# Kernel tuning notes

Hardware: AMD Instinct MI355X
Metric: run time of the kernel (lower is better)

The kernel has to match this reference:

```python
import jax, jax.numpy as jnp
import numpy as np
import math

E_IN, E_OUT = 512, 96
B, QL, PL = 64, 128, 196

def _lin(k, shape):
    fan_in = shape[1]
    bound = 1.0 / math.sqrt(fan_in)
    k1, k2 = jax.random.split(k)
    W = jax.random.uniform(k1, shape, jnp.float32, -bound, bound)
    b = jax.random.uniform(k2, (shape[0],), jnp.float32, -bound, bound)
    return W, b

def setup_inputs() -> dict:
    key = jax.random.key(0)
    ks = jax.random.split(key, 16)
    inp = {
        'z_d_cls': jax.random.normal(ks[0], (B, E_IN), jnp.float32),
        'Z_d_tok': jax.random.normal(ks[1], (B, QL, E_IN), jnp.float32),
        'z_t_cls': jax.random.normal(ks[2], (B, E_IN), jnp.float32),
        'Z_t_tok': jax.random.normal(ks[3], (B, QL, E_IN), jnp.float32),
        'z_v_cls': jax.random.normal(ks[4], (B, E_IN), jnp.float32),
        'Z_v_patch': jax.random.normal(ks[5], (B, PL, E_IN), jnp.float32),
    }
    names = ['t_cls', 'd_cls', 'v_cls', 't_tok', 'v_patch', 'tgl_q', 'tgl_k', 'tgl_v']
    for i, n in enumerate(names):
        W, b = _lin(ks[6 + i], (E_OUT, E_IN))
        inp[f'W_{n}'] = W
        inp[f'b_{n}'] = b
    inp['ln_g'] = jnp.ones((E_OUT,), jnp.float32)
    inp['ln_b'] = jnp.zeros((E_OUT,), jnp.float32)
    return inp

def _l2n(x, eps=1e-6):
    return x / jnp.maximum(jnp.linalg.norm(x, axis=-1, keepdims=True), eps)

def _proj(x, W, b):
    return x @ W.T + b

def _layer_norm(x, g, b, eps=1e-5):
    mu = jnp.mean(x, axis=-1, keepdims=True)
    var = jnp.mean((x - mu) ** 2, axis=-1, keepdims=True)
    return (x - mu) / jnp.sqrt(var + eps) * g + b

def reference(z_d_cls, Z_d_tok, z_t_cls, Z_t_tok, z_v_cls, Z_v_patch,
              W_t_cls, b_t_cls, W_d_cls, b_d_cls, W_v_cls, b_v_cls,
              W_t_tok, b_t_tok, W_v_patch, b_v_patch,
              W_tgl_q, b_tgl_q, W_tgl_k, b_tgl_k, W_tgl_v, b_tgl_v,
              ln_g, ln_b):
    # --- TGG: global-global text/doc cosine sim [B, B]
    t = _l2n(_proj(z_t_cls, W_t_cls, b_t_cls))
    d = _l2n(_proj(z_d_cls, W_d_cls, b_d_cls))
    S_TGG = t @ d.T
    # --- TGL: cross-attention over all batch pairs
    Q = _proj(Z_d_tok, W_tgl_q, b_tgl_q)   # [b, q, h]
    K = _proj(Z_t_tok, W_tgl_k, b_tgl_k)   # [c, k, h]
    V = _proj(Z_t_tok, W_tgl_v, b_tgl_v)   # [c, k, h]
    scores = jnp.einsum('bqh,ckh->bcqk', Q, K) / math.sqrt(E_OUT)
    attn = jax.nn.softmax(scores, axis=-1)
    context = jnp.einsum('bcqk,ckh->bcqh', attn, V).mean(axis=2)  # [b, c, h]
    context = _layer_norm(context, ln_g, ln_b)
    S_TGL = jnp.einsum('ih,ijh->ij', d, _l2n(context))
    S_TIB = 0.5 * (S_TGG + S_TGL)
    # --- CGG: global-global text/vision cosine sim
    v = _l2n(_proj(z_v_cls, W_v_cls, b_v_cls))
    S_CGG = t @ v.T
    # --- CLL: token-patch max similarity
    t_tok = _l2n(_proj(Z_t_tok, W_t_tok, b_t_tok))        # [b, t, h]
    v_pat = _l2n(_proj(Z_v_patch, W_v_patch, b_v_patch))  # [c, p, h]
    sim = jnp.einsum('bth,cph->bctp', t_tok, v_pat)
    S_CLL = sim.max(axis=(-1, -2))
    S_CAB = 0.5 * (S_CGG + S_CLL)
    return S_TIB + S_CAB
```

## Files before the change

kernel.cpp:

```cpp
#include <hip/hip_runtime.h>
#include <hip/hip_bf16.h>
#include <math.h>

typedef __bf16 bf16;
typedef __attribute__((ext_vector_type(8))) __bf16 bf16x8;
typedef __attribute__((ext_vector_type(2))) float f32x2;
typedef __attribute__((ext_vector_type(4))) float f32x4;
typedef __attribute__((ext_vector_type(4))) unsigned int uint4v;

#define MFMA16(a, b, c) __builtin_amdgcn_mfma_f32_16x16x32_bf16(a, b, c, 0, 0, 0)

#define QSCALE 0.14724450f

__device__ inline bf16x8 cvt8(const float* p) {
    f32x4 lo = *(const f32x4*)p;
    f32x4 hi = *(const f32x4*)(p + 4);
    bf16x8 r;
    r[0] = (bf16)lo[0]; r[1] = (bf16)lo[1]; r[2] = (bf16)lo[2]; r[3] = (bf16)lo[3];
    r[4] = (bf16)hi[0]; r[5] = (bf16)hi[1]; r[6] = (bf16)hi[2]; r[7] = (bf16)hi[3];
    return r;
}


struct WPtrs { const float* W[8]; };

__global__ __launch_bounds__(256) void cvtw_kernel(WPtrs wp, bf16* __restrict__ Wb) {
    int j   = blockIdx.x / 48;
    int blk = blockIdx.x - j * 48;
    int idx = (blk * 256 + threadIdx.x) * 4;
    f32x4 v = *(const f32x4*)(wp.W[j] + idx);
    bf16* dst = Wb + j * 49152 + idx;
    dst[0] = (bf16)v[0]; dst[1] = (bf16)v[1]; dst[2] = (bf16)v[2]; dst[3] = (bf16)v[3];
}


struct ProjParams {
    const float* src[8];
    const float* B[8];
    void* dst[8];
    const bf16* Wb;
};

__global__ __launch_bounds__(256) void proj_kernel(ProjParams p) {
    int g   = blockIdx.x;
    int tid = threadIdx.x;
    int w2 = tid >> 6;
    int nh = w2 & 1, kh = w2 >> 1;
    int lane = tid & 63;
    int m = lane & 15, quad = lane >> 4;

    int job = 0, base = 0;
    if (g >= 2)    { job = 1; base = 2; }
    if (g >= 4)    { job = 2; base = 4; }
    if (g >= 6)    { job = 3; base = 6; }
    if (g >= 262)  { job = 4; base = 262; }
    if (g >= 518)  { job = 5; base = 518; }
    if (g >= 774)  { job = 6; base = 774; }
    if (g >= 1030) { job = 7; base = 1030; }
    int r0 = (g - base) << 5;

    const float* X  = p.src[job];
    const bf16*  wb = p.Wb + job * 49152 + (size_t)(nh * 48 + m) * 512 + kh * 256 + quad * 8;
    const float* x0 = X + (size_t)(r0 + m) * 512 + kh * 256 + quad * 8;
    const float* x1 = x0 + 16 * 512;

    f32x4 acc[2][3] = {};
    #pragma unroll
    for (int kk = 0; kk < 256; kk += 32) {
        bf16x8 a0 = cvt8(x0 + kk);
        bf16x8 a1 = cvt8(x1 + kk);
        #pragma unroll
        for (int nt = 0; nt < 3; nt++) {
            bf16x8 b = *(const bf16x8*)(wb + nt * 8192 + kk);
            acc[0][nt] = MFMA16(a0, b, acc[0][nt]);
            acc[1][nt] = MFMA16(a1, b, acc[1][nt]);
        }
    }

    __shared__ float red[2 * 64 * 24];
    __shared__ float sx[2][2][16];
    float* myred = red + (nh * 64 + lane) * 24;
    if (kh) {
        #pragma unroll
        for (int t2 = 0; t2 < 2; t2++)
            #pragma unroll
            for (int nt = 0; nt < 3; nt++)
                *(f32x4*)(myred + (t2 * 3 + nt) * 4) = acc[t2][nt];
    }
    __syncthreads();

    bool norm = (job < 3) || (job >= 6);
    const float* Bv = p.B[job];
    if (!kh) {
        #pragma unroll
        for (int t2 = 0; t2 < 2; t2++)
            #pragma unroll
            for (int nt = 0; nt < 3; nt++) {
                f32x4 o = *(const f32x4*)(myred + (t2 * 3 + nt) * 4);
                float bb = Bv[nh * 48 + nt * 16 + m];
                acc[t2][nt][0] += o[0] + bb; acc[t2][nt][1] += o[1] + bb;
                acc[t2][nt][2] += o[2] + bb; acc[t2][nt][3] += o[3] + bb;
            }
        if (norm) {
            float ss[2][4];
            #pragma unroll
            for (int t2 = 0; t2 < 2; t2++)
                #pragma unroll
                for (int r = 0; r < 4; r++) {
                    float s = 0.0f;
                    #pragma unroll
                    for (int nt = 0; nt < 3; nt++) s += acc[t2][nt][r] * acc[t2][nt][r];
                    s += __shfl_xor(s, 1); s += __shfl_xor(s, 2);
                    s += __shfl_xor(s, 4); s += __shfl_xor(s, 8);
                    ss[t2][r] = s;
                }
            if (m == 0) {
                #pragma unroll
                for (int t2 = 0; t2 < 2; t2++)
                    #pragma unroll
                    for (int r = 0; r < 4; r++)
                        sx[nh][t2][quad * 4 + r] = ss[t2][r];
            }
        }
    }
    __syncthreads();
    if (!kh) {
        if (norm) {
            #pragma unroll
            for (int t2 = 0; t2 < 2; t2++)
                #pragma unroll
                for (int r = 0; r < 4; r++) {
                    float s = 0.0f;
                    #pragma unroll
                    for (int nt = 0; nt < 3; nt++) s += acc[t2][nt][r] * acc[t2][nt][r];
                    s += __shfl_xor(s, 1); s += __shfl_xor(s, 2);
                    s += __shfl_xor(s, 4); s += __shfl_xor(s, 8);
                    float tot = s + sx[1 - nh][t2][quad * 4 + r];
                    float inv = 1.0f / fmaxf(sqrtf(tot), 1e-6f);
                    #pragma unroll
                    for (int nt = 0; nt < 3; nt++) acc[t2][nt][r] *= inv;
                }
        } else if (job == 3) {
            #pragma unroll
            for (int t2 = 0; t2 < 2; t2++)
                #pragma unroll
                for (int nt = 0; nt < 3; nt++) {
                    acc[t2][nt][0] *= QSCALE; acc[t2][nt][1] *= QSCALE;
                    acc[t2][nt][2] *= QSCALE; acc[t2][nt][3] *= QSCALE;
                }
        }
        if (job < 3) {
            float* dst = (float*)p.dst[job];
            #pragma unroll
            for (int t2 = 0; t2 < 2; t2++)
                #pragma unroll
                for (int r = 0; r < 4; r++)
                    #pragma unroll
                    for (int nt = 0; nt < 3; nt++)
                        dst[(size_t)(r0 + t2 * 16 + quad * 4 + r) * 96 + nh * 48 + nt * 16 + m] = acc[t2][nt][r];
        } else {
            bf16* dst = (bf16*)p.dst[job];
            #pragma unroll
            for (int t2 = 0; t2 < 2; t2++)
                #pragma unroll
                for (int r = 0; r < 4; r++)
                    #pragma unroll
                    for (int nt = 0; nt < 3; nt++)
                        dst[(size_t)(r0 + t2 * 16 + quad * 4 + r) * 96 + nh * 48 + nt * 16 + m] = (bf16)acc[t2][nt][r];
        }
    }
}


__global__ __launch_bounds__(256) void attn_kernel(
    const bf16* __restrict__ Qg, const bf16* __restrict__ Kg, const bf16* __restrict__ Vg,
    float* __restrict__ Ctx)
{
    int pr = blockIdx.x;
    int b = pr >> 6, c = pr & 63;
    int tid = threadIdx.x, lane = tid & 63, w = tid >> 6;
    int m = lane & 15, quad = lane >> 4;
    const bf16* Q = Qg + (size_t)b * (128 * 96);
    const bf16* K = Kg + (size_t)c * (128 * 96);
    const bf16* V = Vg + (size_t)c * (128 * 96);

    __shared__ __align__(16) bf16 Klds[128 * 104];
    #pragma unroll
    for (int it = 0; it < 6; it++) {
        int ch = it * 256 + tid;
        int row = ch / 12, seg = ch - row * 12;
        *(uint4v*)(Klds + row * 104 + seg * 8) = *(const uint4v*)(K + ch * 8);
    }
    __syncthreads();

    f32x4 acc[2][8] = {};
    #pragma unroll
    for (int kk = 0; kk < 96; kk += 32) {
        bf16x8 a0 = *(const bf16x8*)(Q + (size_t)(w * 32 + m) * 96 + kk + quad * 8);
        bf16x8 a1 = *(const bf16x8*)(Q + (size_t)(w * 32 + 16 + m) * 96 + kk + quad * 8);
        #pragma unroll
        for (int nt = 0; nt < 8; nt++) {
            bf16x8 bb = *(const bf16x8*)(Klds + (nt * 16 + m) * 104 + kk + quad * 8);
            acc[0][nt] = MFMA16(a0, bb, acc[0][nt]);
            acc[1][nt] = MFMA16(a1, bb, acc[1][nt]);
        }
    }
    float wpart[8];
    #pragma unroll
    for (int nt = 0; nt < 8; nt++) wpart[nt] = 0.0f;
    #pragma unroll
    for (int mt = 0; mt < 2; mt++) {
        #pragma unroll
        for (int r = 0; r < 4; r++) {
            float tv[8]; float s = 0.0f;
            #pragma unroll
            for (int nt = 0; nt < 8; nt++) { tv[nt] = exp2f(acc[mt][nt][r]); s += tv[nt]; }
            s += __shfl_xor(s, 1); s += __shfl_xor(s, 2);
            s += __shfl_xor(s, 4); s += __shfl_xor(s, 8);
            float inv = 1.0f / s;
            #pragma unroll
            for (int nt = 0; nt < 8; nt++) wpart[nt] += tv[nt] * inv;
        }
    }
    #pragma unroll
    for (int nt = 0; nt < 8; nt++) {
        wpart[nt] += __shfl_xor(wpart[nt], 16);
        wpart[nt] += __shfl_xor(wpart[nt], 32);
    }
    __shared__ float wsum4[4][128];
    __shared__ float wk[128];
    __shared__ float ctxp[4][96];
    if (lane < 16) {
        #pragma unroll
        for (int nt = 0; nt < 8; nt++) wsum4[w][nt * 16 + lane] = wpart[nt];
    }
    __syncthreads();
    if (tid < 128) wk[tid] = wsum4[0][tid] + wsum4[1][tid] + wsum4[2][tid] + wsum4[3][tid];
    __syncthreads();
    {
        float c0 = 0.0f, c1 = 0.0f;
        if (lane < 48) {
            #pragma unroll 4
            for (int r = 0; r < 32; r++) {
                int k = w * 32 + r;
                unsigned u = *(const unsigned*)(V + (size_t)k * 96 + lane * 2);
                float lo = __uint_as_float(u << 16);
                float hi = __uint_as_float(u & 0xffff0000u);
                float wkk = wk[k];
                c0 += wkk * lo; c1 += wkk * hi;
            }
            ctxp[w][lane * 2]     = c0;
            ctxp[w][lane * 2 + 1] = c1;
        }
    }
    __syncthreads();
    if (tid < 96)
        Ctx[(size_t)pr * 96 + tid] =
            (ctxp[0][tid] + ctxp[1][tid] + ctxp[2][tid] + ctxp[3][tid]) * (1.0f / 128.0f);
}


__global__ __launch_bounds__(256) void cll_kernel(
    const bf16* __restrict__ Tt, const bf16* __restrict__ Vp,
    const float* __restrict__ Ctx, const float* __restrict__ t,
    const float* __restrict__ d, const float* __restrict__ v,
    const float* __restrict__ ln_g, const float* __restrict__ ln_b,
    float* __restrict__ out)
{
    int c = blockIdx.x >> 3, bg = blockIdx.x & 7;
    int tid = threadIdx.x, lane = tid & 63, w = tid >> 6;
    int m = lane & 15, quad = lane >> 4;
    const bf16* P = Vp + (size_t)c * (196 * 96);

    __shared__ __align__(16) bf16 Plds[196 * 104];
    __shared__ float red[8][4];
    for (int ch = tid; ch < 2352; ch += 256) {
        int row = ch / 12, seg = ch - row * 12;
        *(uint4v*)(Plds + row * 104 + seg * 8) = *(const uint4v*)(P + ch * 8);
    }
    int rofs[13];
    #pragma unroll
    for (int nt = 0; nt < 13; nt++) {
        int r = nt * 16 + m; if (r > 195) r = 195;
        rofs[nt] = r * 104;
    }
    __syncthreads();

    for (int bi = 0; bi < 8; bi++) {
        const bf16* T = Tt + (size_t)(bg * 8 + bi) * (128 * 96);
        f32x4 acc[2][13] = {};
        #pragma unroll
        for (int kk = 0; kk < 96; kk += 32) {
            bf16x8 a0 = *(const bf16x8*)(T + (size_t)(w * 32 + m) * 96 + kk + quad * 8);
            bf16x8 a1 = *(const bf16x8*)(T + (size_t)(w * 32 + 16 + m) * 96 + kk + quad * 8);
            #pragma unroll
            for (int nt = 0; nt < 13; nt++) {
                bf16x8 bb = *(const bf16x8*)(Plds + rofs[nt] + kk + quad * 8);
                acc[0][nt] = MFMA16(a0, bb, acc[0][nt]);
                acc[1][nt] = MFMA16(a1, bb, acc[1][nt]);
            }
        }
        float mx = -3.4e38f;
        #pragma unroll
        for (int mt = 0; mt < 2; mt++)
            #pragma unroll
            for (int nt = 0; nt < 13; nt++)
                #pragma unroll
                for (int r = 0; r < 4; r++) mx = fmaxf(mx, acc[mt][nt][r]);
        #pragma unroll
        for (int dd = 1; dd < 64; dd <<= 1) mx = fmaxf(mx, __shfl_xor(mx, dd));
        if (lane == 0) red[bi][w] = mx;
    }
    __syncthreads();

    #pragma unroll
    for (int half = 0; half < 2; half++) {
        int bi = w + half * 4;
        int i  = bg * 8 + bi;
        int pr = i * 64 + c;
        float scll = fmaxf(fmaxf(red[bi][0], red[bi][1]), fmaxf(red[bi][2], red[bi][3]));
        bool act = lane < 48;
        float c0 = 0, c1 = 0, t0 = 0, t1 = 0;
        float dj0 = 0, dj1 = 0, di0 = 0, di1 = 0, v0 = 0, v1 = 0, g0 = 0, g1 = 0, bb0 = 0, bb1 = 0;
        if (act) {
            f32x2 cc  = *(const f32x2*)(Ctx + (size_t)pr * 96 + lane * 2);
            f32x2 tt  = *(const f32x2*)(t + i * 96 + lane * 2);
            f32x2 ddj = *(const f32x2*)(d + c * 96 + lane * 2);
            f32x2 ddi = *(const f32x2*)(d + i * 96 + lane * 2);
            f32x2 vv  = *(const f32x2*)(v + c * 96 + lane * 2);
            f32x2 gg  = *(const f32x2*)(ln_g + lane * 2);
            f32x2 bbv = *(const f32x2*)(ln_b + lane * 2);
            c0 = cc[0]; c1 = cc[1]; t0 = tt[0]; t1 = tt[1];
            dj0 = ddj[0]; dj1 = ddj[1]; di0 = ddi[0]; di1 = ddi[1];
            v0 = vv[0]; v1 = vv[1];
            g0 = gg[0]; g1 = gg[1]; bb0 = bbv[0]; bb1 = bbv[1];
        }
        float s = c0 + c1;
        #pragma unroll
        for (int k = 1; k < 64; k <<= 1) s += __shfl_xor(s, k);
        float mean = s * (1.0f / 96.0f);
        float e0 = act ? (c0 - mean) : 0.0f;
        float e1 = act ? (c1 - mean) : 0.0f;
        float q = e0 * e0 + e1 * e1;
        #pragma unroll
        for (int k = 1; k < 64; k <<= 1) q += __shfl_xor(q, k);
        float rstd = rsqrtf(q * (1.0f / 96.0f) + 1e-5f);
        float y0 = act ? (e0 * rstd * g0 + bb0) : 0.0f;
        float y1 = act ? (e1 * rstd * g1 + bb1) : 0.0f;
        float dot = y0 * di0 + y1 * di1;
        float ssq = y0 * y0 + y1 * y1;
        float tg  = t0 * dj0 + t1 * dj1;
        float cg  = t0 * v0 + t1 * v1;
        #pragma unroll
        for (int k = 1; k < 64; k <<= 1) {
            dot += __shfl_xor(dot, k); ssq += __shfl_xor(ssq, k);
            tg  += __shfl_xor(tg, k);  cg  += __shfl_xor(cg, k);
        }
        if (lane == 0) {
            float stgl = dot / fmaxf(sqrtf(ssq), 1e-6f);
            out[pr] = 0.5f * (tg + stgl) + 0.5f * (cg + scll);
        }
    }
}


extern "C" void kernel_launch(void* const* d_in, const int* in_sizes, int n_in,
                              void* d_out, int out_size, void* d_ws, size_t ws_size,
                              hipStream_t stream)
{
    (void)in_sizes; (void)n_in; (void)out_size; (void)ws_size;
    char* ws = (char*)d_ws;
    float* t     = (float*)(ws + 0);
    float* d     = (float*)(ws + 24576);
    float* v     = (float*)(ws + 49152);
    bf16* Wb = (bf16*)(ws + 106496);
    bf16* Qb = (bf16*)(ws + 892928);
    bf16* Kb = (bf16*)(ws + 892928 + 1572864);
    bf16* Vb = (bf16*)(ws + 892928 + 2 * 1572864);
    bf16* Tt = (bf16*)(ws + 892928 + 3 * 1572864);
    bf16* Vp = (bf16*)(ws + 892928 + 4 * 1572864);
    float* Ctx = (float*)(ws + 892928 + 4 * 1572864 + 2408448);

    WPtrs wp;
    wp.W[0] = (const float*)d_in[6];
    wp.W[1] = (const float*)d_in[8];
    wp.W[2] = (const float*)d_in[10];
    wp.W[3] = (const float*)d_in[16];
    wp.W[4] = (const float*)d_in[18];
    wp.W[5] = (const float*)d_in[20];
    wp.W[6] = (const float*)d_in[12];
    wp.W[7] = (const float*)d_in[14];
    hipLaunchKernelGGL(cvtw_kernel, dim3(384), dim3(256), 0, stream, wp, Wb);

    ProjParams pp;
    pp.Wb = Wb;
    pp.src[0] = (const float*)d_in[2];  pp.B[0] = (const float*)d_in[7];  pp.dst[0] = t;
    pp.src[1] = (const float*)d_in[0];  pp.B[1] = (const float*)d_in[9];  pp.dst[1] = d;
    pp.src[2] = (const float*)d_in[4];  pp.B[2] = (const float*)d_in[11]; pp.dst[2] = v;
    pp.src[3] = (const float*)d_in[1];  pp.B[3] = (const float*)d_in[17]; pp.dst[3] = Qb;
    pp.src[4] = (const float*)d_in[3];  pp.B[4] = (const float*)d_in[19]; pp.dst[4] = Kb;
    pp.src[5] = (const float*)d_in[3];  pp.B[5] = (const float*)d_in[21]; pp.dst[5] = Vb;
    pp.src[6] = (const float*)d_in[3];  pp.B[6] = (const float*)d_in[13]; pp.dst[6] = Tt;
    pp.src[7] = (const float*)d_in[5];  pp.B[7] = (const float*)d_in[15]; pp.dst[7] = Vp;
    hipLaunchKernelGGL(proj_kernel, dim3(1422), dim3(256), 0, stream, pp);

    hipLaunchKernelGGL(attn_kernel, dim3(4096), dim3(256), 0, stream,
                       (const bf16*)Qb, (const bf16*)Kb, (const bf16*)Vb, Ctx);
    hipLaunchKernelGGL(cll_kernel, dim3(512), dim3(256), 0, stream,
                       (const bf16*)Tt, (const bf16*)Vp,
                       (const float*)Ctx, (const float*)t, (const float*)d, (const float*)v,
                       (const float*)d_in[22], (const float*)d_in[23], (float*)d_out);
}
```

Baseline: 238.4 us.

## Restructure projection kernel with LDS-staged inputs and fused K/V/Tt projections

Rewrites the projection kernel to stage fp32 input rows into a double-buffered, XOR-swizzled LDS tile with async global-to-LDS loads. The K, V and token projections of Z_t_tok now share one pass over that input, so it is read once instead of three times. The split-K reduction through shared memory is replaced by a row split across waves. This cuts global traffic and block count, at the cost of more accumulator registers for the fused path and extra barriers per chunk.

Result: no change. 240.2 us (+0.8%).

```diff
diff --git a/kernel.cpp b/kernel.cpp
--- a/kernel.cpp
+++ b/kernel.cpp
@@ -12,9 +12,13 @@
 
 #define QSCALE 0.14724450f
 
-__device__ inline bf16x8 cvt8(const float* p) {
-    f32x4 lo = *(const f32x4*)p;
-    f32x4 hi = *(const f32x4*)(p + 4);
+__device__ __forceinline__ void async16(void* lds, const void* g) {
+    __builtin_amdgcn_global_load_lds(
+        (const __attribute__((address_space(1))) unsigned int*)g,
+        (__attribute__((address_space(3))) unsigned int*)lds, 16, 0, 0);
+}
+
+__device__ __forceinline__ bf16x8 cvt8v(f32x4 lo, f32x4 hi) {
     bf16x8 r;
     r[0] = (bf16)lo[0]; r[1] = (bf16)lo[1]; r[2] = (bf16)lo[2]; r[3] = (bf16)lo[3];
     r[4] = (bf16)hi[0]; r[5] = (bf16)hi[1]; r[6] = (bf16)hi[2]; r[7] = (bf16)hi[3];
@@ -41,133 +45,132 @@
     const bf16* Wb;
 };
 
-__global__ __launch_bounds__(256) void proj_kernel(ProjParams p) {
-    int g   = blockIdx.x;
-    int tid = threadIdx.x;
-    int w2 = tid >> 6;
-    int nh = w2 & 1, kh = w2 >> 1;
-    int lane = tid & 63;
+__device__ __forceinline__ void stageX(const float* X, int r0, int c, char* dstb,
+                                       int w4, int lane) {
+    #pragma unroll
+    for (int it = 0; it < 4; it++) {
+        int bidx = it * 256 + w4 * 64;
+        int idx  = bidx + lane;
+        int row  = idx >> 5, sp = idx & 31;
+        int sl   = sp ^ (row & 15);
+        async16(dstb + (size_t)bidx * 16,
+                X + (size_t)(r0 + row) * 512 + c * 128 + sl * 4);
+    }
+}
+
+template<int NSUB, bool F32OUT>
+__device__ __forceinline__ void proj_body(
+    const float* __restrict__ X, int r0, const bf16* __restrict__ Wj,
+    const float* B0, const float* B1, const float* B2,
+    void* D0, void* D1, void* D2,
+    int normMask, float scale,
+    char* Xp, float (*sx)[2][32], int tid)
+{
+    int w4 = tid >> 6, lane = tid & 63;
+    int nh = w4 & 1, rh = w4 >> 1;
     int m = lane & 15, quad = lane >> 4;
 
-    int job = 0, base = 0;
-    if (g >= 2)    { job = 1; base = 2; }
-    if (g >= 4)    { job = 2; base = 4; }
-    if (g >= 6)    { job = 3; base = 6; }
-    if (g >= 262)  { job = 4; base = 262; }
-    if (g >= 518)  { job = 5; base = 518; }
-    if (g >= 774)  { job = 6; base = 774; }
-    if (g >= 1030) { job = 7; base = 1030; }
-    int r0 = (g - base) << 5;
-
-    const float* X  = p.src[job];
-    const bf16*  wb = p.Wb + job * 49152 + (size_t)(nh * 48 + m) * 512 + kh * 256 + quad * 8;
-    const float* x0 = X + (size_t)(r0 + m) * 512 + kh * 256 + quad * 8;
-    const float* x1 = x0 + 16 * 512;
-
-    f32x4 acc[2][3] = {};
-    #pragma unroll
-    for (int kk = 0; kk < 256; kk += 32) {
-        bf16x8 a0 = cvt8(x0 + kk);
-        bf16x8 a1 = cvt8(x1 + kk);
+    const bf16* wbL = Wj + (size_t)(nh * 48 + m) * 512 + quad * 8;
+
+    f32x4 acc[3 * NSUB] = {};
+
+    stageX(X, r0, 0, Xp, w4, lane);
+    __syncthreads();
+    #pragma unroll
+    for (int c = 0; c < 4; c++) {
+        int bb = c & 1;
+        if (c < 3) stageX(X, r0, c + 1, Xp + (bb ^ 1) * 16384, w4, lane);
+        const char* xb = Xp + bb * 16384 + (rh * 16 + m) * 512;
+        #pragma unroll
+        for (int kkk = 0; kkk < 4; kkk++) {
+            int sl = kkk * 8 + quad * 2;
+            f32x4 lo = *(const f32x4*)(xb + ((sl ^ m) * 16));
+            f32x4 hi = *(const f32x4*)(xb + (((sl + 1) ^ m) * 16));
+            bf16x8 a = cvt8v(lo, hi);
+            const bf16* wk = wbL + c * 128 + kkk * 32;
+            #pragma unroll
+            for (int j = 0; j < NSUB; j++)
+                #pragma unroll
+                for (int nt = 0; nt < 3; nt++)
+                    acc[j * 3 + nt] = MFMA16(a, *(const bf16x8*)(wk + j * 49152 + nt * 8192),
+                                             acc[j * 3 + nt]);
+        }
+        __syncthreads();
+    }
+
+    float ss[NSUB][4];
+    #pragma unroll
+    for (int j = 0; j < NSUB; j++) {
+        const float* Bj = (j == 0) ? B0 : ((j == 1) ? B1 : B2);
         #pragma unroll
         for (int nt = 0; nt < 3; nt++) {
-            bf16x8 b = *(const bf16x8*)(wb + nt * 8192 + kk);
-            acc[0][nt] = MFMA16(a0, b, acc[0][nt]);
-            acc[1][nt] = MFMA16(a1, b, acc[1][nt]);
-        }
-    }
-
-    __shared__ float red[2 * 64 * 24];
-    __shared__ float sx[2][2][16];
-    float* myred = red + (nh * 64 + lane) * 24;
-    if (kh) {
-        #pragma unroll
-        for (int t2 = 0; t2 < 2; t2++)
-            #pragma unroll
-            for (int nt = 0; nt < 3; nt++)
-                *(f32x4*)(myred + (t2 * 3 + nt) * 4) = acc[t2][nt];
-    }
-    __syncthreads();
-
-    bool norm = (job < 3) || (job >= 6);
-    const float* Bv = p.B[job];
-    if (!kh) {
-        #pragma unroll
-        for (int t2 = 0; t2 < 2; t2++)
-            #pragma unroll
-            for (int nt = 0; nt < 3; nt++) {
-                f32x4 o = *(const f32x4*)(myred + (t2 * 3 + nt) * 4);
-                float bb = Bv[nh * 48 + nt * 16 + m];
-                acc[t2][nt][0] += o[0] + bb; acc[t2][nt][1] += o[1] + bb;
-                acc[t2][nt][2] += o[2] + bb; acc[t2][nt][3] += o[3] + bb;
-            }
-        if (norm) {
-            float ss[2][4];
-            #pragma unroll
-            for (int t2 = 0; t2 < 2; t2++)
+            float bv = Bj[nh * 48 + nt * 16 + m];
+            #pragma unroll
+            for (int r = 0; r < 4; r++)
+                acc[j * 3 + nt][r] = (acc[j * 3 + nt][r] + bv) * scale;
+        }
+        if ((normMask >> j) & 1) {
+            #pragma unroll
+            for (int r = 0; r < 4; r++) {
+                float s = 0.0f;
                 #pragma unroll
-                for (int r = 0; r < 4; r++) {
-                    float s = 0.0f;
-                    #pragma unroll
-                    for (int nt = 0; nt < 3; nt++) s += acc[t2][nt][r] * acc[t2][nt][r];
-                    s += __shfl_xor(s, 1); s += __shfl_xor(s, 2);
-                    s += __shfl_xor(s, 4); s += __shfl_xor(s, 8);
-                    ss[t2][r] = s;
-                }
+                for (int nt = 0; nt < 3; nt++) s += acc[j * 3 + nt][r] * acc[j * 3 + nt][r];
+                s += __shfl_xor(s, 1); s += __shfl_xor(s, 2);
+                s += __shfl_xor(s, 4); s += __shfl_xor(s, 8);
+                ss[j][r] = s;
+            }
             if (m == 0) {
                 #pragma unroll
-                for (int t2 = 0; t2 < 2; t2++)
-                    #pragma unroll
-                    for (int r = 0; r < 4; r++)
-                        sx[nh][t2][quad * 4 + r] = ss[t2][r];
-            }
-        }
-    }
-    __syncthreads();
-    if (!kh) {
-        if (norm) {
-            #pragma unroll
-            for (int t2 = 0; t2 < 2; t2++)
+                for (int r = 0; r < 4; r++)
+                    sx[j][nh][rh * 16 + quad * 4 + r] = ss[j][r];
+            }
+        }
+    }
+    __syncthreads();
+    #pragma unroll
+    for (int j = 0; j < NSUB; j++) {
+        if ((normMask >> j) & 1) {
+            #pragma unroll
+            for (int r = 0; r < 4; r++) {
+                float tot = ss[j][r] + sx[j][1 - nh][rh * 16 + quad * 4 + r];
+                float inv = 1.0f / fmaxf(sqrtf(tot), 1e-6f);
                 #pragma unroll
-                for (int r = 0; r < 4; r++) {
-                    float s = 0.0f;
-                    #pragma unroll
-                    for (int nt = 0; nt < 3; nt++) s += acc[t2][nt][r] * acc[t2][nt][r];
-                    s += __shfl_xor(s, 1); s += __shfl_xor(s, 2);
-                    s += __shfl_xor(s, 4); s += __shfl_xor(s, 8);
-                    float tot = s + sx[1 - nh][t2][quad * 4 + r];
-                    float inv = 1.0f / fmaxf(sqrtf(tot), 1e-6f);
-                    #pragma unroll
-                    for (int nt = 0; nt < 3; nt++) acc[t2][nt][r] *= inv;
-                }
-        } else if (job == 3) {
-            #pragma unroll
-            for (int t2 = 0; t2 < 2; t2++)
-                #pragma unroll
-                for (int nt = 0; nt < 3; nt++) {
-                    acc[t2][nt][0] *= QSCALE; acc[t2][nt][1] *= QSCALE;
-                    acc[t2][nt][2] *= QSCALE; acc[t2][nt][3] *= QSCALE;
-                }
-        }
-        if (job < 3) {
-            float* dst = (float*)p.dst[job];
-            #pragma unroll
-            for (int t2 = 0; t2 < 2; t2++)
-                #pragma unroll
-                for (int r = 0; r < 4; r++)
-                    #pragma unroll
-                    for (int nt = 0; nt < 3; nt++)
-                        dst[(size_t)(r0 + t2 * 16 + quad * 4 + r) * 96 + nh * 48 + nt * 16 + m] = acc[t2][nt][r];
-        } else {
-            bf16* dst = (bf16*)p.dst[job];
-            #pragma unroll
-            for (int t2 = 0; t2 < 2; t2++)
-                #pragma unroll
-                for (int r = 0; r < 4; r++)
-                    #pragma unroll
-                    for (int nt = 0; nt < 3; nt++)
-                        dst[(size_t)(r0 + t2 * 16 + quad * 4 + r) * 96 + nh * 48 + nt * 16 + m] = (bf16)acc[t2][nt][r];
-        }
+                for (int nt = 0; nt < 3; nt++) acc[j * 3 + nt][r] *= inv;
+            }
+        }
+        void* Dj = (j == 0) ? D0 : ((j == 1) ? D1 : D2);
+        #pragma unroll
+        for (int nt = 0; nt < 3; nt++)
+            #pragma unroll
+            for (int r = 0; r < 4; r++) {
+                size_t o = (size_t)(r0 + rh * 16 + quad * 4 + r) * 96 + nh * 48 + nt * 16 + m;
+                if constexpr (F32OUT) ((float*)Dj)[o] = acc[j * 3 + nt][r];
+                else                  ((bf16*)Dj)[o] = (bf16)acc[j * 3 + nt][r];
+            }
+    }
+}
+
+__global__ __launch_bounds__(256) void proj_kernel(ProjParams p) {
+    __shared__ __align__(16) char Xp[32768];
+    __shared__ float sx[3][2][32];
+    int g = blockIdx.x, tid = threadIdx.x;
+    if (g < 256) {
+        proj_body<3, false>(p.src[4], g << 5, p.Wb + 4 * 49152,
+                            p.B[4], p.B[5], p.B[6], p.dst[4], p.dst[5], p.dst[6],
+                            4, 1.0f, Xp, sx, tid);
+    } else if (g < 512) {
+        proj_body<1, false>(p.src[3], (g - 256) << 5, p.Wb + 3 * 49152,
+                            p.B[3], 0, 0, p.dst[3], 0, 0,
+                            0, QSCALE, Xp, sx, tid);
+    } else if (g < 904) {
+        proj_body<1, false>(p.src[7], (g - 512) << 5, p.Wb + 7 * 49152,
+                            p.B[7], 0, 0, p.dst[7], 0, 0,
+                            1, 1.0f, Xp, sx, tid);
+    } else {
+        int jb = (g - 904) >> 1;
+        proj_body<1, true>(p.src[jb], ((g - 904) & 1) << 5, p.Wb + jb * 49152,
+                           p.B[jb], 0, 0, p.dst[jb], 0, 0,
+                           1, 1.0f, Xp, sx, tid);
     }
 }
 
@@ -402,7 +405,7 @@
     pp.src[5] = (const float*)d_in[3];  pp.B[5] = (const float*)d_in[21]; pp.dst[5] = Vb;
     pp.src[6] = (const float*)d_in[3];  pp.B[6] = (const float*)d_in[13]; pp.dst[6] = Tt;
     pp.src[7] = (const float*)d_in[5];  pp.B[7] = (const float*)d_in[15]; pp.dst[7] = Vp;
-    hipLaunchKernelGGL(proj_kernel, dim3(1422), dim3(256), 0, stream, pp);
+    hipLaunchKernelGGL(proj_kernel, dim3(910), dim3(256), 0, stream, pp);
 
     hipLaunchKernelGGL(attn_kernel, dim3(4096), dim3(256), 0, stream,
                        (const bf16*)Qb, (const bf16*)Kb, (const bf16*)Vb, Ctx);
```

## Give each wavefront a full 32-row projection tile, dropping LDS reductions

Applied to the files above, without the earlier changes.

The projection kernel now assigns one independent 32x96 output tile with the full K=512 reduction to each wavefront, where before four waves split N and K and combined partial sums through shared memory. This removes the LDS reduction, both block barriers and the cross-half norm exchange, and cuts the grid from 1422 to 356 blocks. In exchange each wave holds twice as many accumulators and serially runs twice as many MFMAs. The small CLS jobs are moved to the end of the wave index space, and bias plus Q scaling are folded into one pass.

New measurement: 240.7 us. No clear change (+1.0%).

```diff
diff --git a/kernel.cpp b/kernel.cpp
--- a/kernel.cpp
+++ b/kernel.cpp
@@ -12,9 +12,7 @@
 
 #define QSCALE 0.14724450f
 
-__device__ inline bf16x8 cvt8(const float* p) {
-    f32x4 lo = *(const f32x4*)p;
-    f32x4 hi = *(const f32x4*)(p + 4);
+__device__ __forceinline__ bf16x8 cvt8v(f32x4 lo, f32x4 hi) {
     bf16x8 r;
     r[0] = (bf16)lo[0]; r[1] = (bf16)lo[1]; r[2] = (bf16)lo[2]; r[3] = (bf16)lo[3];
     r[4] = (bf16)hi[0]; r[5] = (bf16)hi[1]; r[6] = (bf16)hi[2]; r[7] = (bf16)hi[3];
@@ -42,132 +40,87 @@
 };
 
 __global__ __launch_bounds__(256) void proj_kernel(ProjParams p) {
-    int g   = blockIdx.x;
-    int tid = threadIdx.x;
-    int w2 = tid >> 6;
-    int nh = w2 & 1, kh = w2 >> 1;
-    int lane = tid & 63;
+    int w = threadIdx.x >> 6, lane = threadIdx.x & 63;
+    int gw = blockIdx.x * 4 + w;
     int m = lane & 15, quad = lane >> 4;
 
-    int job = 0, base = 0;
-    if (g >= 2)    { job = 1; base = 2; }
-    if (g >= 4)    { job = 2; base = 4; }
-    if (g >= 6)    { job = 3; base = 6; }
-    if (g >= 262)  { job = 4; base = 262; }
-    if (g >= 518)  { job = 5; base = 518; }
-    if (g >= 774)  { job = 6; base = 774; }
-    if (g >= 1030) { job = 7; base = 1030; }
-    int r0 = (g - base) << 5;
-
-    const float* X  = p.src[job];
-    const bf16*  wb = p.Wb + job * 49152 + (size_t)(nh * 48 + m) * 512 + kh * 256 + quad * 8;
-    const float* x0 = X + (size_t)(r0 + m) * 512 + kh * 256 + quad * 8;
-    const float* x1 = x0 + 16 * 512;
-
-    f32x4 acc[2][3] = {};
-    #pragma unroll
-    for (int kk = 0; kk < 256; kk += 32) {
-        bf16x8 a0 = cvt8(x0 + kk);
-        bf16x8 a1 = cvt8(x1 + kk);
-        #pragma unroll
-        for (int nt = 0; nt < 3; nt++) {
-            bf16x8 b = *(const bf16x8*)(wb + nt * 8192 + kk);
+    int job, t0;
+    if      (gw < 256)  { job = 3; t0 = gw; }
+    else if (gw < 512)  { job = 4; t0 = gw - 256; }
+    else if (gw < 768)  { job = 5; t0 = gw - 512; }
+    else if (gw < 1024) { job = 6; t0 = gw - 768; }
+    else if (gw < 1416) { job = 7; t0 = gw - 1024; }
+    else if (gw < 1422) { int r = gw - 1416; job = r >> 1; t0 = r & 1; }
+    else return;
+    int r0 = t0 << 5;
+
+    const float* X = p.src[job] + (size_t)(r0 + m) * 512 + quad * 8;
+    const bf16*  W = p.Wb + job * 49152 + (size_t)m * 512 + quad * 8;
+
+    f32x4 acc[2][6] = {};
+    #pragma unroll
+    for (int kk = 0; kk < 512; kk += 32) {
+        bf16x8 a0 = cvt8v(*(const f32x4*)(X + kk),
+                          *(const f32x4*)(X + kk + 4));
+        bf16x8 a1 = cvt8v(*(const f32x4*)(X + 16 * 512 + kk),
+                          *(const f32x4*)(X + 16 * 512 + kk + 4));
+        #pragma unroll
+        for (int nt = 0; nt < 6; nt++) {
+            bf16x8 b = *(const bf16x8*)(W + (size_t)nt * 16 * 512 + kk);
             acc[0][nt] = MFMA16(a0, b, acc[0][nt]);
             acc[1][nt] = MFMA16(a1, b, acc[1][nt]);
         }
     }
 
-    __shared__ float red[2 * 64 * 24];
-    __shared__ float sx[2][2][16];
-    float* myred = red + (nh * 64 + lane) * 24;
-    if (kh) {
-        #pragma unroll
-        for (int t2 = 0; t2 < 2; t2++)
-            #pragma unroll
-            for (int nt = 0; nt < 3; nt++)
-                *(f32x4*)(myred + (t2 * 3 + nt) * 4) = acc[t2][nt];
-    }
-    __syncthreads();
-
-    bool norm = (job < 3) || (job >= 6);
+    bool  norm  = (job < 3) || (job >= 6);
+    float scale = (job == 3) ? QSCALE : 1.0f;
     const float* Bv = p.B[job];
-    if (!kh) {
-        #pragma unroll
-        for (int t2 = 0; t2 < 2; t2++)
-            #pragma unroll
-            for (int nt = 0; nt < 3; nt++) {
-                f32x4 o = *(const f32x4*)(myred + (t2 * 3 + nt) * 4);
-                float bb = Bv[nh * 48 + nt * 16 + m];
-                acc[t2][nt][0] += o[0] + bb; acc[t2][nt][1] += o[1] + bb;
-                acc[t2][nt][2] += o[2] + bb; acc[t2][nt][3] += o[3] + bb;
+    float bb[6];
+    #pragma unroll
+    for (int nt = 0; nt < 6; nt++) bb[nt] = Bv[nt * 16 + m];
+
+    #pragma unroll
+    for (int rt = 0; rt < 2; rt++)
+        #pragma unroll
+        for (int nt = 0; nt < 6; nt++)
+            #pragma unroll
+            for (int r = 0; r < 4; r++)
+                acc[rt][nt][r] = (acc[rt][nt][r] + bb[nt]) * scale;
+
+    if (norm) {
+        #pragma unroll
+        for (int rt = 0; rt < 2; rt++)
+            #pragma unroll
+            for (int r = 0; r < 4; r++) {
+                float s = 0.0f;
+                #pragma unroll
+                for (int nt = 0; nt < 6; nt++) s += acc[rt][nt][r] * acc[rt][nt][r];
+                s += __shfl_xor(s, 1); s += __shfl_xor(s, 2);
+                s += __shfl_xor(s, 4); s += __shfl_xor(s, 8);
+                float inv = 1.0f / fmaxf(sqrtf(s), 1e-6f);
+                #pragma unroll
+                for (int nt = 0; nt < 6; nt++) acc[rt][nt][r] *= inv;
             }
-        if (norm) {
-            float ss[2][4];
-            #pragma unroll
-            for (int t2 = 0; t2 < 2; t2++)
-                #pragma unroll
-                for (int r = 0; r < 4; r++) {
-                    float s = 0.0f;
-                    #pragma unroll
-                    for (int nt = 0; nt < 3; nt++) s += acc[t2][nt][r] * acc[t2][nt][r];
-                    s += __shfl_xor(s, 1); s += __shfl_xor(s, 2);
-                    s += __shfl_xor(s, 4); s += __shfl_xor(s, 8);
-                    ss[t2][r] = s;
-                }
-            if (m == 0) {
-                #pragma unroll
-                for (int t2 = 0; t2 < 2; t2++)
-                    #pragma unroll
-                    for (int r = 0; r < 4; r++)
-                        sx[nh][t2][quad * 4 + r] = ss[t2][r];
-            }
-        }
-    }
-    __syncthreads();
-    if (!kh) {
-        if (norm) {
-            #pragma unroll
-            for (int t2 = 0; t2 < 2; t2++)
-                #pragma unroll
-                for (int r = 0; r < 4; r++) {
-                    float s = 0.0f;
-                    #pragma unroll
-                    for (int nt = 0; nt < 3; nt++) s += acc[t2][nt][r] * acc[t2][nt][r];
-                    s += __shfl_xor(s, 1); s += __shfl_xor(s, 2);
-                    s += __shfl_xor(s, 4); s += __shfl_xor(s, 8);
-                    float tot = s + sx[1 - nh][t2][quad * 4 + r];
-                    float inv = 1.0f / fmaxf(sqrtf(tot), 1e-6f);
-                    #pragma unroll
-                    for (int nt = 0; nt < 3; nt++) acc[t2][nt][r] *= inv;
-                }
-        } else if (job == 3) {
-            #pragma unroll
-            for (int t2 = 0; t2 < 2; t2++)
-                #pragma unroll
-                for (int nt = 0; nt < 3; nt++) {
-                    acc[t2][nt][0] *= QSCALE; acc[t2][nt][1] *= QSCALE;
-                    acc[t2][nt][2] *= QSCALE; acc[t2][nt][3] *= QSCALE;
-                }
-        }
-        if (job < 3) {
-            float* dst = (float*)p.dst[job];
-            #pragma unroll
-            for (int t2 = 0; t2 < 2; t2++)
-                #pragma unroll
-                for (int r = 0; r < 4; r++)
-                    #pragma unroll
-                    for (int nt = 0; nt < 3; nt++)
-                        dst[(size_t)(r0 + t2 * 16 + quad * 4 + r) * 96 + nh * 48 + nt * 16 + m] = acc[t2][nt][r];
-        } else {
-            bf16* dst = (bf16*)p.dst[job];
-            #pragma unroll
-            for (int t2 = 0; t2 < 2; t2++)
-                #pragma unroll
-                for (int r = 0; r < 4; r++)
-                    #pragma unroll
-                    for (int nt = 0; nt < 3; nt++)
-                        dst[(size_t)(r0 + t2 * 16 + quad * 4 + r) * 96 + nh * 48 + nt * 16 + m] = (bf16)acc[t2][nt][r];
-        }
+    }
+
+    if (job < 3) {
+        float* dst = (float*)p.dst[job];
+        #pragma unroll
+        for (int rt = 0; rt < 2; rt++)
+            #pragma unroll
+            for (int r = 0; r < 4; r++)
+                #pragma unroll
+                for (int nt = 0; nt < 6; nt++)
+                    dst[(size_t)(r0 + rt * 16 + quad * 4 + r) * 96 + nt * 16 + m] = acc[rt][nt][r];
+    } else {
+        bf16* dst = (bf16*)p.dst[job];
+        #pragma unroll
+        for (int rt = 0; rt < 2; rt++)
+            #pragma unroll
+            for (int r = 0; r < 4; r++)
+                #pragma unroll
+                for (int nt = 0; nt < 6; nt++)
+                    dst[(size_t)(r0 + rt * 16 + quad * 4 + r) * 96 + nt * 16 + m] = (bf16)acc[rt][nt][r];
     }
 }
 
@@ -402,7 +355,7 @@
     pp.src[5] = (const float*)d_in[3];  pp.B[5] = (const float*)d_in[21]; pp.dst[5] = Vb;
     pp.src[6] = (const float*)d_in[3];  pp.B[6] = (const float*)d_in[13]; pp.dst[6] = Tt;
     pp.src[7] = (const float*)d_in[5];  pp.B[7] = (const float*)d_in[15]; pp.dst[7] = Vp;
-    hipLaunchKernelGGL(proj_kernel, dim3(1422), dim3(256), 0, stream, pp);
+    hipLaunchKernelGGL(proj_kernel, dim3(356), dim3(256), 0, stream, pp);
 
     hipLaunchKernelGGL(attn_kernel, dim3(4096), dim3(256), 0, stream,
                        (const bf16*)Qb, (const bf16*)Kb, (const bf16*)Vb, Ctx);
```
